# Optimization experiments

Measured on AMD Instinct MI355X. Metric: run time of the kernel, lower is better.

The kernel has to match this reference:

```python
import jax, jax.numpy as jnp
import numpy as np

UNITS = 1024
NEG_INF = -10000.0


def setup_inputs() -> dict:
    key = jax.random.key(0)
    ks = jax.random.split(key, 5)
    B, S, D = 8, 2048, 1024
    scale = 0.02  # truncated-normal stddev in original init
    x = jax.random.normal(ks[0], (B, S, D), dtype=jnp.float32)
    mask = jax.random.randint(ks[1], (B, S), 0, 2, dtype=jnp.int32)
    Wq = jax.random.normal(ks[2], (D, UNITS), dtype=jnp.float32) * scale
    Wk = jax.random.normal(ks[3], (D, UNITS), dtype=jnp.float32) * scale
    Wv = jax.random.normal(ks[4], (D, UNITS), dtype=jnp.float32) * scale
    bq = jnp.zeros((UNITS,), jnp.float32)
    bk = jnp.zeros((UNITS,), jnp.float32)
    bv = jnp.zeros((UNITS,), jnp.float32)
    return {"x": x, "mask": mask, "Wq": Wq, "bq": bq, "Wk": Wk, "bk": bk, "Wv": Wv, "bv": bv}


def reference(x, mask, Wq, bq, Wk, bk, Wv, bv):
    # Q/K/V projections: [B,S,D] @ [D,U] -> [B,S,U]
    q = jnp.einsum('bsd,du->bsu', x, Wq) + bq
    k = jnp.einsum('bsd,du->bsu', x, Wk) + bk
    v = jnp.einsum('bsd,du->bsu', x, Wv) + bv
    # scaled dot-product scores: [B,S,S]
    scores = jnp.einsum('bqu,bku->bqk', q, k) / jnp.sqrt(jnp.float32(UNITS))
    m = mask.astype(jnp.float32)
    attn_mask = jnp.einsum('bq,bk->bqk', m, m)  # outer-product padding mask
    scores = scores + (1.0 - attn_mask) * NEG_INF
    probs = jax.nn.softmax(scores, axis=-1)
    # dropout is inactive at inference (training=None/False in Keras)
    context = jnp.einsum('bqk,bku->bqu', probs, v)
    return context
```

## Files before the change

kernel.cpp:

```cpp
#include <hip/hip_runtime.h>
#include <stdint.h>

typedef unsigned short u16;
typedef __bf16 bf16x8 __attribute__((ext_vector_type(8)));
typedef float f32x4 __attribute__((ext_vector_type(4)));
typedef unsigned short u16x8 __attribute__((ext_vector_type(8)));
typedef unsigned short u16x4 __attribute__((ext_vector_type(4)));

#define B_BATCH 8
#define S_LEN   2048
#define D_DIM   1024
#define U_DIM   1024

#define BM 128
#define BN 128
#define BK 64

__device__ __forceinline__ float bf2f(u16 h) {
    union { unsigned u; float f; } c; c.u = ((unsigned)h) << 16; return c.f;
}
__device__ __forceinline__ u16 f2bf(float f) {
    union { float f; unsigned u; } c; c.f = f;
    unsigned r = c.u + 0x7fffu + ((c.u >> 16) & 1u);
    return (u16)(r >> 16);
}

__device__ __forceinline__ void cp16(u16* lds, const u16* g) {
    __builtin_amdgcn_global_load_lds((__attribute__((address_space(1))) void*)g,
                                     (__attribute__((address_space(3))) void*)lds,
                                     16, 0, 0);
}

__device__ __forceinline__ void gemm_core(
    const u16* __restrict__ A, int lda,
    const u16* __restrict__ Bt, int ldb,
    int m0, int n0, int K,
    u16* As, u16* Bs, int tid, f32x4 acc[4][4])
{
    const int lane = tid & 63;
    const int wm = ((tid >> 6) >> 1) * 64;
    const int wn = ((tid >> 6) & 1) * 64;
    const int lm = lane & 15;
    const int lq = lane >> 4;
    const int sw = lm & 7;

    for (int k0 = 0; k0 < K; k0 += BK) {
        __syncthreads();
        #pragma unroll
        for (int s = 0; s < 4; ++s) {
            const int c = tid + 256 * s;
            const int r = c >> 3;
            const int q = (c & 7) ^ ((c >> 3) & 7);
            cp16(As + c * 8, A + (long long)(m0 + r) * lda + k0 + q * 8);
            cp16(Bs + c * 8, Bt + (long long)(n0 + r) * ldb + k0 + q * 8);
        }
        __syncthreads();

        #pragma unroll
        for (int ks = 0; ks < 2; ++ks) {
            const int kq = ks * 4 + lq;
            bf16x8 af[4], bfr[4];
            #pragma unroll
            for (int i = 0; i < 4; ++i)
                af[i] = *(const bf16x8*)(As + (wm + i * 16 + lm) * BK + (kq ^ sw) * 8);
            #pragma unroll
            for (int j = 0; j < 4; ++j)
                bfr[j] = *(const bf16x8*)(Bs + (wn + j * 16 + lm) * BK + (kq ^ sw) * 8);
            #pragma unroll
            for (int i = 0; i < 4; ++i)
                #pragma unroll
                for (int j = 0; j < 4; ++j)
                    acc[i][j] = __builtin_amdgcn_mfma_f32_16x16x32_bf16(af[i], bfr[j], acc[i][j], 0, 0, 0);
        }
    }
}

__device__ __forceinline__ void swizzle_mnz(int ph, int& mi, int& ni, int& z) {
    const int lid = blockIdx.x + gridDim.x * (blockIdx.y + gridDim.y * blockIdx.z);
    z = lid & 7;
    const int t = lid >> 3;
    const int ntn = gridDim.x;
    const int panel = t / (ph * ntn);
    const int r = t - panel * (ph * ntn);
    mi = panel * ph + (r % ph);
    ni = r / ph;
}

__global__ __launch_bounds__(256) void prep(
    const float* __restrict__ x, u16* __restrict__ xb,
    const float* __restrict__ Wq, const float* __restrict__ Wk,
    const float* __restrict__ Wv, u16* __restrict__ WT,
    float* __restrict__ rowsum)
{
    __shared__ u16 tile[32][33];
    const int b = blockIdx.x;
    const int tid = threadIdx.x;
    if (b < 16384) {
        const int i = b * 256 + tid;
        float4 v = ((const float4*)x)[i];
        ushort4 o;
        o.x = f2bf(v.x); o.y = f2bf(v.y); o.z = f2bf(v.z); o.w = f2bf(v.w);
        ((ushort4*)xb)[i] = o;
    } else if (b < 16384 + 3072) {
        const int b2 = b - 16384;
        const int w = b2 >> 10;
        const int idx = b2 & 1023;
        const float* src = (w == 0) ? Wq : (w == 1) ? Wk : Wv;
        u16* dst = WT + (size_t)w * D_DIM * U_DIM;
        const int c0 = (idx & 31) * 32, rr0 = (idx >> 5) * 32;
        const int tx = tid & 31, ty = tid >> 5;
        #pragma unroll
        for (int i = 0; i < 32; i += 8)
            tile[ty + i][tx] = f2bf(src[(long long)(rr0 + ty + i) * U_DIM + c0 + tx]);
        __syncthreads();
        #pragma unroll
        for (int i = 0; i < 32; i += 8)
            dst[(long long)(c0 + ty + i) * D_DIM + rr0 + tx] = tile[tx][ty + i];
    } else {
        const int i = (b - 16384 - 3072) * 256 + tid;
        float4 z4; z4.x = z4.y = z4.z = z4.w = 0.0f;
        ((float4*)rowsum)[i] = z4;
    }
}

__global__ __launch_bounds__(256, 2) void qkv_proj(
    const u16* __restrict__ xb, const u16* __restrict__ WT,
    const float* __restrict__ bq, const float* __restrict__ bk,
    const float* __restrict__ bv,
    u16* __restrict__ Q, u16* __restrict__ Ko, u16* __restrict__ VT)
{
    __shared__ __align__(16) u16 smem[BM * BK * 2];
    u16* As = smem;
    u16* Bs = smem + BM * BK;

    const int tgt = blockIdx.x >> 3;
    const int n0 = (blockIdx.x & 7) * BN;
    const int m0 = blockIdx.y * BM;
    const int tid = threadIdx.x;
    const int lane = tid & 63;
    const int wm = ((tid >> 6) >> 1) * 64;
    const int wn = ((tid >> 6) & 1) * 64;

    const u16* Bt = WT + (size_t)tgt * (D_DIM * U_DIM);
    const float* bias = (tgt == 0) ? bq : (tgt == 1) ? bk : bv;

    f32x4 acc[4][4] = {};
    gemm_core(xb, D_DIM, Bt, D_DIM, m0, n0, D_DIM, As, Bs, tid, acc);

    const int col = lane & 15;
    const int rb  = (lane >> 4) * 4;

    if (tgt < 2) {
        u16* C = (tgt == 0) ? Q : Ko;
        #pragma unroll
        for (int j = 0; j < 4; ++j) {
            const int n = n0 + wn + j * 16 + col;
            const float bvv = bias[n];
            #pragma unroll
            for (int i = 0; i < 4; ++i) {
                const long long mr = m0 + wm + i * 16 + rb;
                #pragma unroll
                for (int r = 0; r < 4; ++r)
                    C[(mr + r) * U_DIM + n] = f2bf(acc[i][j][r] + bvv);
            }
        }
    } else {
        __syncthreads();
        #pragma unroll
        for (int j = 0; j < 4; ++j) {
            const int cl = wn + j * 16 + col;
            const float bvv = bias[n0 + cl];
            #pragma unroll
            for (int i = 0; i < 4; ++i) {
                const int rowb = wm + i * 16 + rb;
                u16x4 pk;
                #pragma unroll
                for (int r = 0; r < 4; ++r) pk[r] = f2bf(acc[i][j][r] + bvv);
                const int idx = cl * 128 + (((rowb >> 3) ^ (cl & 15)) * 8) + (rowb & 7);
                *(u16x4*)(smem + idx) = pk;
            }
        }
        __syncthreads();
        const int zb = m0 >> 11;
        const int s0 = m0 & 2047;
        u16* VTg = VT + (size_t)zb * ((size_t)S_LEN * U_DIM);
        #pragma unroll
        for (int s = 0; s < 8; ++s) {
            const int cid = tid + 256 * s;
            const int cl = cid >> 4;
            const int m8 = cid & 15;
            u16x8 v = *(const u16x8*)(smem + cl * 128 + ((m8 ^ (cl & 15)) * 8));
            *(u16x8*)(VTg + (size_t)(n0 + cl) * S_LEN + s0 + m8 * 8) = v;
        }
    }
}

__global__ __launch_bounds__(256, 2) void scores_exp(
    const u16* __restrict__ Qb, const u16* __restrict__ Kb,
    u16* __restrict__ E, const int* __restrict__ mask,
    float* __restrict__ rowsum, int ph)
{
    __shared__ __align__(16) u16 smem[BM * BK * 2];
    u16* As = smem;
    u16* Bs = smem + BM * BK;

    int mi, ni, z;
    swizzle_mnz(ph, mi, ni, z);
    const int m0 = mi * BM, n0 = ni * BN;
    const long long SU = (long long)S_LEN * U_DIM;
    const long long SS = (long long)S_LEN * S_LEN;

    const int tid = threadIdx.x;
    const int lane = tid & 63;
    const int wm = ((tid >> 6) >> 1) * 64;
    const int wn = ((tid >> 6) & 1) * 64;

    f32x4 acc[4][4] = {};
    gemm_core(Qb + (long long)z * SU, U_DIM, Kb + (long long)z * SU, U_DIM,
              m0, n0, U_DIM, As, Bs, tid, acc);

    u16* Eg = E + (long long)z * SS;
    const int* mrow = mask + (size_t)z * S_LEN;
    const int col = lane & 15;
    const int rb  = (lane >> 4) * 4;

    int mj[4];
    #pragma unroll
    for (int j = 0; j < 4; ++j) mj[j] = mrow[n0 + wn + j * 16 + col];

    #pragma unroll
    for (int i = 0; i < 4; ++i) {
        #pragma unroll
        for (int r = 0; r < 4; ++r) {
            const int row = m0 + wm + i * 16 + rb + r;
            const int mi_ = mrow[row];
            float partial = 0.0f;
            #pragma unroll
            for (int j = 0; j < 4; ++j) {
                float e = (mi_ && !mj[j]) ? 0.0f : __expf(acc[i][j][r] * 0.03125f);
                const u16 h = f2bf(e);
                Eg[(long long)row * S_LEN + n0 + wn + j * 16 + col] = h;
                partial += bf2f(h);
            }
            partial += __shfl_xor(partial, 1, 64);
            partial += __shfl_xor(partial, 2, 64);
            partial += __shfl_xor(partial, 4, 64);
            partial += __shfl_xor(partial, 8, 64);
            if ((lane & 15) == 0)
                atomicAdd(&rowsum[(size_t)z * S_LEN + row], partial);
        }
    }
}

__global__ __launch_bounds__(256, 2) void pv_gemm(
    const u16* __restrict__ E, const u16* __restrict__ VT,
    float* __restrict__ out, const float* __restrict__ rowsum, int ph)
{
    __shared__ __align__(16) u16 smem[BM * BK * 2];
    u16* As = smem;
    u16* Bs = smem + BM * BK;

    int mi, ni, z;
    swizzle_mnz(ph, mi, ni, z);
    const int m0 = mi * BM, n0 = ni * BN;
    const long long SU = (long long)S_LEN * U_DIM;
    const long long SS = (long long)S_LEN * S_LEN;

    const int tid = threadIdx.x;
    const int lane = tid & 63;
    const int wm = ((tid >> 6) >> 1) * 64;
    const int wn = ((tid >> 6) & 1) * 64;

    f32x4 acc[4][4] = {};
    gemm_core(E + (long long)z * SS, S_LEN, VT + (long long)z * SU, S_LEN,
              m0, n0, S_LEN, As, Bs, tid, acc);

    float* Cg = out + (long long)z * SU;
    const float* rs = rowsum + (size_t)z * S_LEN;
    const int col = lane & 15;
    const int rb  = (lane >> 4) * 4;

    #pragma unroll
    for (int i = 0; i < 4; ++i) {
        #pragma unroll
        for (int r = 0; r < 4; ++r) {
            const int row = m0 + wm + i * 16 + rb + r;
            const float inv = 1.0f / rs[row];
            #pragma unroll
            for (int j = 0; j < 4; ++j)
                Cg[(long long)row * U_DIM + n0 + wn + j * 16 + col] = acc[i][j][r] * inv;
        }
    }
}

extern "C" void kernel_launch(void* const* d_in, const int* in_sizes, int n_in,
                              void* d_out, int out_size, void* d_ws, size_t ws_size,
                              hipStream_t stream)
{
    (void)in_sizes; (void)n_in; (void)out_size; (void)ws_size;
    const float* x    = (const float*)d_in[0];
    const int*   mask = (const int*)d_in[1];
    const float* Wq   = (const float*)d_in[2];
    const float* bq   = (const float*)d_in[3];
    const float* Wk   = (const float*)d_in[4];
    const float* bk   = (const float*)d_in[5];
    const float* Wv   = (const float*)d_in[6];
    const float* bv   = (const float*)d_in[7];

    const size_t DU  = (size_t)D_DIM * U_DIM;
    const size_t BSU = (size_t)B_BATCH * S_LEN * U_DIM;

    u16* ws  = (u16*)d_ws;
    u16* Qb  = ws;
    u16* Kb  = Qb + BSU;
    u16* VTb = Kb + BSU;
    u16* WT  = VTb + BSU;
    float* rowsum = (float*)(WT + 3 * DU);
    u16* E   = (u16*)(rowsum + (size_t)B_BATCH * S_LEN);
    u16* xb  = E;

    dim3 blk(256);

    prep<<<dim3(16384 + 3072 + 16), blk, 0, stream>>>(x, xb, Wq, Wk, Wv, WT, rowsum);

    qkv_proj<<<dim3(24, 128), blk, 0, stream>>>(xb, WT, bq, bk, bv, Qb, Kb, VTb);

    scores_exp<<<dim3(S_LEN / BN, S_LEN / BM, B_BATCH), blk, 0, stream>>>(
        Qb, Kb, E, mask, rowsum, 8);

    pv_gemm<<<dim3(U_DIM / BN, S_LEN / BM, B_BATCH), blk, 0, stream>>>(
        E, VTb, (float*)d_out, rowsum, 16);
}
```

Baseline: 281.1 us.

## Switch GEMMs to 256x256 tiles with 8 waves and double-buffered LDS prefetch

Replaces the 128x128 single-buffered GEMM core with a 256x256-tile, 512-thread version used by all three GEMM kernels. It double-buffers the K tiles in LDS, issuing the next tile's global-to-LDS copies while the current MFMA quarters run. It splits each k-step into four MFMA quadrants separated by raw barriers and raises wave priority during the MFMA bursts. The larger tile cuts global and LDS traffic per FLOP. In exchange it uses 128KB of LDS and 128 accumulator registers per thread, which limits residency to one block per CU, and the smaller grids (256 blocks for pv_gemm) may leave load imbalance.

```diff
diff --git a/kernel.cpp b/kernel.cpp
--- a/kernel.cpp
+++ b/kernel.cpp
@@ -12,9 +12,10 @@
 #define D_DIM   1024
 #define U_DIM   1024
 
-#define BM 128
-#define BN 128
 #define BK 64
+#define HALF_U16  16384
+#define TILE_U16  32768
+#define LDS_U16   65536
 
 __device__ __forceinline__ float bf2f(u16 h) {
     union { unsigned u; float f; } c; c.u = ((unsigned)h) << 16; return c.f;
@@ -31,47 +32,106 @@
                                      16, 0, 0);
 }
 
-__device__ __forceinline__ void gemm_core(
+__device__ __forceinline__ void barrier_raw() { asm volatile("s_barrier" ::: "memory"); }
+
+__device__ __forceinline__ void stage4(u16* __restrict__ dst, const u16* __restrict__ src,
+                                       int ld, int row0, int kc, int tid) {
+    #pragma unroll
+    for (int s = 0; s < 4; ++s) {
+        const int c = tid + 512 * s;
+        const int r = c >> 3;
+        const int q = (c & 7) ^ (r & 7);
+        cp16(dst + c * 8, src + (long long)(row0 + r) * ld + kc + q * 8);
+    }
+}
+
+__device__ __forceinline__ void ldsA8(bf16x8* a, const u16* __restrict__ T,
+                                      int rbase, int lm, int lq, int sw) {
+    #pragma unroll
+    for (int i = 0; i < 4; ++i)
+        #pragma unroll
+        for (int ks = 0; ks < 2; ++ks)
+            a[i * 2 + ks] = *(const bf16x8*)(T + (rbase + i * 16 + lm) * BK + (((ks * 4 + lq) ^ sw) * 8));
+}
+__device__ __forceinline__ void ldsB4(bf16x8* b, const u16* __restrict__ T,
+                                      int rbase, int lm, int lq, int sw) {
+    #pragma unroll
+    for (int j = 0; j < 2; ++j)
+        #pragma unroll
+        for (int ks = 0; ks < 2; ++ks)
+            b[j * 2 + ks] = *(const bf16x8*)(T + (rbase + j * 16 + lm) * BK + (((ks * 4 + lq) ^ sw) * 8));
+}
+
+template<int I0, int J0>
+__device__ __forceinline__ void mmaq(f32x4 (*acc)[4], const bf16x8* a, const bf16x8* b) {
+    __builtin_amdgcn_s_setprio(1);
+    #pragma unroll
+    for (int i = 0; i < 4; ++i)
+        #pragma unroll
+        for (int j = 0; j < 2; ++j)
+            #pragma unroll
+            for (int ks = 0; ks < 2; ++ks)
+                acc[I0 + i][J0 + j] = __builtin_amdgcn_mfma_f32_16x16x32_bf16(
+                    a[i * 2 + ks], b[j * 2 + ks], acc[I0 + i][J0 + j], 0, 0, 0);
+    __builtin_amdgcn_s_setprio(0);
+    __builtin_amdgcn_sched_barrier(0);
+}
+
+__device__ __forceinline__ void gemm256(
     const u16* __restrict__ A, int lda,
     const u16* __restrict__ Bt, int ldb,
     int m0, int n0, int K,
-    u16* As, u16* Bs, int tid, f32x4 acc[4][4])
+    u16* lds, int tid, f32x4 (*acc)[4])
 {
     const int lane = tid & 63;
-    const int wm = ((tid >> 6) >> 1) * 64;
-    const int wn = ((tid >> 6) & 1) * 64;
-    const int lm = lane & 15;
-    const int lq = lane >> 4;
-    const int sw = lm & 7;
-
-    for (int k0 = 0; k0 < K; k0 += BK) {
-        __syncthreads();
-        #pragma unroll
-        for (int s = 0; s < 4; ++s) {
-            const int c = tid + 256 * s;
-            const int r = c >> 3;
-            const int q = (c & 7) ^ ((c >> 3) & 7);
-            cp16(As + c * 8, A + (long long)(m0 + r) * lda + k0 + q * 8);
-            cp16(Bs + c * 8, Bt + (long long)(n0 + r) * ldb + k0 + q * 8);
-        }
-        __syncthreads();
-
-        #pragma unroll
-        for (int ks = 0; ks < 2; ++ks) {
-            const int kq = ks * 4 + lq;
-            bf16x8 af[4], bfr[4];
-            #pragma unroll
-            for (int i = 0; i < 4; ++i)
-                af[i] = *(const bf16x8*)(As + (wm + i * 16 + lm) * BK + (kq ^ sw) * 8);
-            #pragma unroll
-            for (int j = 0; j < 4; ++j)
-                bfr[j] = *(const bf16x8*)(Bs + (wn + j * 16 + lm) * BK + (kq ^ sw) * 8);
-            #pragma unroll
-            for (int i = 0; i < 4; ++i)
-                #pragma unroll
-                for (int j = 0; j < 4; ++j)
-                    acc[i][j] = __builtin_amdgcn_mfma_f32_16x16x32_bf16(af[i], bfr[j], acc[i][j], 0, 0, 0);
-        }
+    const int wid  = tid >> 6;
+    const int wmh  = (wid >> 2) * 128;
+    const int wnh  = (wid & 3) * 64;
+    const int lm   = lane & 15;
+    const int lq   = lane >> 4;
+    const int sw   = lm & 7;
+
+    stage4(lds,            A,  lda, m0, 0, tid);
+    stage4(lds + HALF_U16, Bt, ldb, n0, 0, tid);
+    asm volatile("s_waitcnt vmcnt(0)" ::: "memory");
+    barrier_raw();
+
+    const int NT = K >> 6;
+    int buf = 0;
+    for (int kt = 0; kt < NT; ++kt) {
+        const u16* As  = lds + buf * TILE_U16;
+        const u16* Bs  = As + HALF_U16;
+        u16* Asn = lds + (buf ^ 1) * TILE_U16;
+        u16* Bsn = Asn + HALF_U16;
+        const int kn = (kt + 1) << 6;
+        const bool pre = (kt + 1) < NT;
+        bf16x8 a[8], b[4];
+
+        ldsA8(a, As, wmh, lm, lq, sw);
+        ldsB4(b, Bs, wnh, lm, lq, sw);
+        if (pre) stage4(Asn, A, lda, m0, kn, tid);
+        barrier_raw();
+        mmaq<0, 0>(acc, a, b);
+        barrier_raw();
+
+        ldsB4(b, Bs, wnh + 32, lm, lq, sw);
+        if (pre) stage4(Bsn, Bt, ldb, n0, kn, tid);
+        barrier_raw();
+        mmaq<0, 2>(acc, a, b);
+        barrier_raw();
+
+        ldsA8(a, As, wmh + 64, lm, lq, sw);
+        barrier_raw();
+        mmaq<4, 2>(acc, a, b);
+        barrier_raw();
+
+        ldsB4(b, Bs, wnh, lm, lq, sw);
+        if (pre) asm volatile("s_waitcnt vmcnt(0)" ::: "memory");
+        barrier_raw();
+        mmaq<4, 0>(acc, a, b);
+        barrier_raw();
+
+        buf ^= 1;
     }
 }
 
@@ -123,42 +183,36 @@
     }
 }
 
-__global__ __launch_bounds__(256, 2) void qkv_proj(
+__global__ __launch_bounds__(512, 2) void qkv_proj(
     const u16* __restrict__ xb, const u16* __restrict__ WT,
     const float* __restrict__ bq, const float* __restrict__ bk,
     const float* __restrict__ bv,
     u16* __restrict__ Q, u16* __restrict__ Ko, u16* __restrict__ VT)
 {
-    __shared__ __align__(16) u16 smem[BM * BK * 2];
-    u16* As = smem;
-    u16* Bs = smem + BM * BK;
-
-    const int tgt = blockIdx.x >> 3;
-    const int n0 = (blockIdx.x & 7) * BN;
-    const int m0 = blockIdx.y * BM;
+    __shared__ __align__(16) u16 smem[LDS_U16];
+    const int tgt = blockIdx.x >> 2;
+    const int n0 = (blockIdx.x & 3) * 256;
+    const int m0 = blockIdx.y * 256;
     const int tid = threadIdx.x;
-    const int lane = tid & 63;
-    const int wm = ((tid >> 6) >> 1) * 64;
-    const int wn = ((tid >> 6) & 1) * 64;
+    const int lane = tid & 63, wid = tid >> 6;
+    const int wmh = (wid >> 2) * 128, wnh = (wid & 3) * 64;
+    const int lm = lane & 15, lq = lane >> 4;
 
     const u16* Bt = WT + (size_t)tgt * (D_DIM * U_DIM);
     const float* bias = (tgt == 0) ? bq : (tgt == 1) ? bk : bv;
 
-    f32x4 acc[4][4] = {};
-    gemm_core(xb, D_DIM, Bt, D_DIM, m0, n0, D_DIM, As, Bs, tid, acc);
-
-    const int col = lane & 15;
-    const int rb  = (lane >> 4) * 4;
+    f32x4 acc[8][4] = {};
+    gemm256(xb, D_DIM, Bt, D_DIM, m0, n0, D_DIM, smem, tid, acc);
 
     if (tgt < 2) {
         u16* C = (tgt == 0) ? Q : Ko;
         #pragma unroll
         for (int j = 0; j < 4; ++j) {
-            const int n = n0 + wn + j * 16 + col;
+            const int n = n0 + wnh + j * 16 + lm;
             const float bvv = bias[n];
             #pragma unroll
-            for (int i = 0; i < 4; ++i) {
-                const long long mr = m0 + wm + i * 16 + rb;
+            for (int i = 0; i < 8; ++i) {
+                const long long mr = m0 + wmh + i * 16 + lq * 4;
                 #pragma unroll
                 for (int r = 0; r < 4; ++r)
                     C[(mr + r) * U_DIM + n] = f2bf(acc[i][j][r] + bvv);
@@ -168,15 +222,15 @@
         __syncthreads();
         #pragma unroll
         for (int j = 0; j < 4; ++j) {
-            const int cl = wn + j * 16 + col;
+            const int cl = wnh + j * 16 + lm;
             const float bvv = bias[n0 + cl];
             #pragma unroll
-            for (int i = 0; i < 4; ++i) {
-                const int rowb = wm + i * 16 + rb;
+            for (int i = 0; i < 8; ++i) {
+                const int rowb = wmh + i * 16 + lq * 4;
                 u16x4 pk;
                 #pragma unroll
                 for (int r = 0; r < 4; ++r) pk[r] = f2bf(acc[i][j][r] + bvv);
-                const int idx = cl * 128 + (((rowb >> 3) ^ (cl & 15)) * 8) + (rowb & 7);
+                const int idx = cl * 256 + (((rowb >> 3) ^ (cl & 31)) * 8) + (rowb & 7);
                 *(u16x4*)(smem + idx) = pk;
             }
         }
@@ -185,110 +239,102 @@
         const int s0 = m0 & 2047;
         u16* VTg = VT + (size_t)zb * ((size_t)S_LEN * U_DIM);
         #pragma unroll
-        for (int s = 0; s < 8; ++s) {
-            const int cid = tid + 256 * s;
-            const int cl = cid >> 4;
-            const int m8 = cid & 15;
-            u16x8 v = *(const u16x8*)(smem + cl * 128 + ((m8 ^ (cl & 15)) * 8));
+        for (int s = 0; s < 16; ++s) {
+            const int cid = tid + 512 * s;
+            const int cl = cid >> 5;
+            const int m8 = cid & 31;
+            u16x8 v = *(const u16x8*)(smem + cl * 256 + ((m8 ^ (cl & 31)) * 8));
             *(u16x8*)(VTg + (size_t)(n0 + cl) * S_LEN + s0 + m8 * 8) = v;
         }
     }
 }
 
-__global__ __launch_bounds__(256, 2) void scores_exp(
+__global__ __launch_bounds__(512, 2) void scores_exp(
     const u16* __restrict__ Qb, const u16* __restrict__ Kb,
     u16* __restrict__ E, const int* __restrict__ mask,
     float* __restrict__ rowsum, int ph)
 {
-    __shared__ __align__(16) u16 smem[BM * BK * 2];
-    u16* As = smem;
-    u16* Bs = smem + BM * BK;
+    __shared__ __align__(16) u16 smem[LDS_U16];
 
     int mi, ni, z;
     swizzle_mnz(ph, mi, ni, z);
-    const int m0 = mi * BM, n0 = ni * BN;
+    const int m0 = mi * 256, n0 = ni * 256;
     const long long SU = (long long)S_LEN * U_DIM;
     const long long SS = (long long)S_LEN * S_LEN;
 
     const int tid = threadIdx.x;
-    const int lane = tid & 63;
-    const int wm = ((tid >> 6) >> 1) * 64;
-    const int wn = ((tid >> 6) & 1) * 64;
-
-    f32x4 acc[4][4] = {};
-    gemm_core(Qb + (long long)z * SU, U_DIM, Kb + (long long)z * SU, U_DIM,
-              m0, n0, U_DIM, As, Bs, tid, acc);
+    const int lane = tid & 63, wid = tid >> 6;
+    const int wmh = (wid >> 2) * 128, wnh = (wid & 3) * 64;
+    const int lm = lane & 15, lq = lane >> 4;
+
+    f32x4 acc[8][4] = {};
+    gemm256(Qb + (long long)z * SU, U_DIM, Kb + (long long)z * SU, U_DIM,
+            m0, n0, U_DIM, smem, tid, acc);
 
     u16* Eg = E + (long long)z * SS;
     const int* mrow = mask + (size_t)z * S_LEN;
-    const int col = lane & 15;
-    const int rb  = (lane >> 4) * 4;
 
     int mj[4];
     #pragma unroll
-    for (int j = 0; j < 4; ++j) mj[j] = mrow[n0 + wn + j * 16 + col];
-
-    #pragma unroll
-    for (int i = 0; i < 4; ++i) {
+    for (int j = 0; j < 4; ++j) mj[j] = mrow[n0 + wnh + j * 16 + lm];
+
+    #pragma unroll
+    for (int i = 0; i < 8; ++i) {
         #pragma unroll
         for (int r = 0; r < 4; ++r) {
-            const int row = m0 + wm + i * 16 + rb + r;
+            const int row = m0 + wmh + i * 16 + lq * 4 + r;
             const int mi_ = mrow[row];
             float partial = 0.0f;
             #pragma unroll
             for (int j = 0; j < 4; ++j) {
                 float e = (mi_ && !mj[j]) ? 0.0f : __expf(acc[i][j][r] * 0.03125f);
                 const u16 h = f2bf(e);
-                Eg[(long long)row * S_LEN + n0 + wn + j * 16 + col] = h;
+                Eg[(long long)row * S_LEN + n0 + wnh + j * 16 + lm] = h;
                 partial += bf2f(h);
             }
             partial += __shfl_xor(partial, 1, 64);
             partial += __shfl_xor(partial, 2, 64);
             partial += __shfl_xor(partial, 4, 64);
             partial += __shfl_xor(partial, 8, 64);
-            if ((lane & 15) == 0)
+            if (lm == 0)
                 atomicAdd(&rowsum[(size_t)z * S_LEN + row], partial);
         }
     }
 }
 
-__global__ __launch_bounds__(256, 2) void pv_gemm(
+__global__ __launch_bounds__(512, 2) void pv_gemm(
     const u16* __restrict__ E, const u16* __restrict__ VT,
     float* __restrict__ out, const float* __restrict__ rowsum, int ph)
 {
-    __shared__ __align__(16) u16 smem[BM * BK * 2];
-    u16* As = smem;
-    u16* Bs = smem + BM * BK;
+    __shared__ __align__(16) u16 smem[LDS_U16];
 
     int mi, ni, z;
     swizzle_mnz(ph, mi, ni, z);
-    const int m0 = mi * BM, n0 = ni * BN;
+    const int m0 = mi * 256, n0 = ni * 256;
     const long long SU = (long long)S_LEN * U_DIM;
     const long long SS = (long long)S_LEN * S_LEN;
 
     const int tid = threadIdx.x;
-    const int lane = tid & 63;
-    const int wm = ((tid >> 6) >> 1) * 64;
-    const int wn = ((tid >> 6) & 1) * 64;
-
-    f32x4 acc[4][4] = {};
-    gemm_core(E + (long long)z * SS, S_LEN, VT + (long long)z * SU, S_LEN,
-              m0, n0, S_LEN, As, Bs, tid, acc);
+    const int lane = tid & 63, wid = tid >> 6;
+    const int wmh = (wid >> 2) * 128, wnh = (wid & 3) * 64;
+    const int lm = lane & 15, lq = lane >> 4;
+
+    f32x4 acc[8][4] = {};
+    gemm256(E + (long long)z * SS, S_LEN, VT + (long long)z * SU, S_LEN,
+            m0, n0, S_LEN, smem, tid, acc);
 
     float* Cg = out + (long long)z * SU;
     const float* rs = rowsum + (size_t)z * S_LEN;
-    const int col = lane & 15;
-    const int rb  = (lane >> 4) * 4;
-
-    #pragma unroll
-    for (int i = 0; i < 4; ++i) {
+
+    #pragma unroll
+    for (int i = 0; i < 8; ++i) {
         #pragma unroll
         for (int r = 0; r < 4; ++r) {
-            const int row = m0 + wm + i * 16 + rb + r;
+            const int row = m0 + wmh + i * 16 + lq * 4 + r;
             const float inv = 1.0f / rs[row];
             #pragma unroll
             for (int j = 0; j < 4; ++j)
-                Cg[(long long)row * U_DIM + n0 + wn + j * 16 + col] = acc[i][j][r] * inv;
+                Cg[(long long)row * U_DIM + n0 + wnh + j * 16 + lm] = acc[i][j][r] * inv;
         }
     }
 }
@@ -319,15 +365,11 @@
     u16* E   = (u16*)(rowsum + (size_t)B_BATCH * S_LEN);
     u16* xb  = E;
 
-    dim3 blk(256);
-
-    prep<<<dim3(16384 + 3072 + 16), blk, 0, stream>>>(x, xb, Wq, Wk, Wv, WT, rowsum);
-
-    qkv_proj<<<dim3(24, 128), blk, 0, stream>>>(xb, WT, bq, bk, bv, Qb, Kb, VTb);
-
-    scores_exp<<<dim3(S_LEN / BN, S_LEN / BM, B_BATCH), blk, 0, stream>>>(
-        Qb, Kb, E, mask, rowsum, 8);
-
-    pv_gemm<<<dim3(U_DIM / BN, S_LEN / BM, B_BATCH), blk, 0, stream>>>(
-        E, VTb, (float*)d_out, rowsum, 16);
-}
+    prep<<<dim3(16384 + 3072 + 16), dim3(256), 0, stream>>>(x, xb, Wq, Wk, Wv, WT, rowsum);
+
+    qkv_proj<<<dim3(12, 64), dim3(512), 0, stream>>>(xb, WT, bq, bk, bv, Qb, Kb, VTb);
+
+    scores_exp<<<dim3(8, 8, 8), dim3(512), 0, stream>>>(Qb, Kb, E, mask, rowsum, 8);
+
+    pv_gemm<<<dim3(4, 8, 8), dim3(512), 0, stream>>>(E, VTb, (float*)d_out, rowsum, 8);
+}
```

Measured after the change: 290.1 us. 1.03x slower.

## Enlarge GEMM block tile to 256x128 with 128-row warp tiles

Applied to the files above, without the earlier changes.

Doubles the M dimension of the block tile across all three GEMM kernels, so each wave computes a 128x64 sub-tile with 8x4 MFMA accumulators. The aim is to raise arithmetic intensity and reuse of the B fragments, cutting LDS and global traffic per FLOP. The V-transpose epilogue now goes through shared memory in two halves because the staging buffer holds only half the tile, and the swizzle panel height is adjusted. In exchange, accumulator registers double and the grid halves, which risks lower occupancy and spills.

```diff
diff --git a/kernel.cpp b/kernel.cpp
--- a/kernel.cpp
+++ b/kernel.cpp
@@ -12,7 +12,7 @@
 #define D_DIM   1024
 #define U_DIM   1024
 
-#define BM 128
+#define BM 256
 #define BN 128
 #define BK 64
 
@@ -35,10 +35,10 @@
     const u16* __restrict__ A, int lda,
     const u16* __restrict__ Bt, int ldb,
     int m0, int n0, int K,
-    u16* As, u16* Bs, int tid, f32x4 acc[4][4])
+    u16* As, u16* Bs, int tid, f32x4 acc[8][4])
 {
     const int lane = tid & 63;
-    const int wm = ((tid >> 6) >> 1) * 64;
+    const int wm = ((tid >> 6) >> 1) * 128;
     const int wn = ((tid >> 6) & 1) * 64;
     const int lm = lane & 15;
     const int lq = lane >> 4;
@@ -47,11 +47,17 @@
     for (int k0 = 0; k0 < K; k0 += BK) {
         __syncthreads();
         #pragma unroll
+        for (int s = 0; s < 8; ++s) {
+            const int c = tid + 256 * s;
+            const int r = c >> 3;
+            const int q = (c & 7) ^ (r & 7);
+            cp16(As + c * 8, A + (long long)(m0 + r) * lda + k0 + q * 8);
+        }
+        #pragma unroll
         for (int s = 0; s < 4; ++s) {
             const int c = tid + 256 * s;
             const int r = c >> 3;
-            const int q = (c & 7) ^ ((c >> 3) & 7);
-            cp16(As + c * 8, A + (long long)(m0 + r) * lda + k0 + q * 8);
+            const int q = (c & 7) ^ (r & 7);
             cp16(Bs + c * 8, Bt + (long long)(n0 + r) * ldb + k0 + q * 8);
         }
         __syncthreads();
@@ -59,18 +65,17 @@
         #pragma unroll
         for (int ks = 0; ks < 2; ++ks) {
             const int kq = ks * 4 + lq;
-            bf16x8 af[4], bfr[4];
-            #pragma unroll
-            for (int i = 0; i < 4; ++i)
-                af[i] = *(const bf16x8*)(As + (wm + i * 16 + lm) * BK + (kq ^ sw) * 8);
+            bf16x8 bfr[4];
             #pragma unroll
             for (int j = 0; j < 4; ++j)
-                bfr[j] = *(const bf16x8*)(Bs + (wn + j * 16 + lm) * BK + (kq ^ sw) * 8);
-            #pragma unroll
-            for (int i = 0; i < 4; ++i)
+                bfr[j] = *(const bf16x8*)(Bs + (wn + j * 16 + lm) * BK + ((kq ^ sw) * 8));
+            #pragma unroll
+            for (int i = 0; i < 8; ++i) {
+                const bf16x8 af = *(const bf16x8*)(As + (wm + i * 16 + lm) * BK + ((kq ^ sw) * 8));
                 #pragma unroll
                 for (int j = 0; j < 4; ++j)
-                    acc[i][j] = __builtin_amdgcn_mfma_f32_16x16x32_bf16(af[i], bfr[j], acc[i][j], 0, 0, 0);
+                    acc[i][j] = __builtin_amdgcn_mfma_f32_16x16x32_bf16(af, bfr[j], acc[i][j], 0, 0, 0);
+            }
         }
     }
 }
@@ -129,7 +134,7 @@
     const float* __restrict__ bv,
     u16* __restrict__ Q, u16* __restrict__ Ko, u16* __restrict__ VT)
 {
-    __shared__ __align__(16) u16 smem[BM * BK * 2];
+    __shared__ __align__(16) u16 smem[(BM + BN) * BK];
     u16* As = smem;
     u16* Bs = smem + BM * BK;
 
@@ -138,13 +143,13 @@
     const int m0 = blockIdx.y * BM;
     const int tid = threadIdx.x;
     const int lane = tid & 63;
-    const int wm = ((tid >> 6) >> 1) * 64;
+    const int wm = ((tid >> 6) >> 1) * 128;
     const int wn = ((tid >> 6) & 1) * 64;
 
     const u16* Bt = WT + (size_t)tgt * (D_DIM * U_DIM);
     const float* bias = (tgt == 0) ? bq : (tgt == 1) ? bk : bv;
 
-    f32x4 acc[4][4] = {};
+    f32x4 acc[8][4] = {};
     gemm_core(xb, D_DIM, Bt, D_DIM, m0, n0, D_DIM, As, Bs, tid, acc);
 
     const int col = lane & 15;
@@ -157,7 +162,7 @@
             const int n = n0 + wn + j * 16 + col;
             const float bvv = bias[n];
             #pragma unroll
-            for (int i = 0; i < 4; ++i) {
+            for (int i = 0; i < 8; ++i) {
                 const long long mr = m0 + wm + i * 16 + rb;
                 #pragma unroll
                 for (int r = 0; r < 4; ++r)
@@ -165,32 +170,38 @@
             }
         }
     } else {
-        __syncthreads();
-        #pragma unroll
-        for (int j = 0; j < 4; ++j) {
-            const int cl = wn + j * 16 + col;
-            const float bvv = bias[n0 + cl];
-            #pragma unroll
-            for (int i = 0; i < 4; ++i) {
-                const int rowb = wm + i * 16 + rb;
-                u16x4 pk;
-                #pragma unroll
-                for (int r = 0; r < 4; ++r) pk[r] = f2bf(acc[i][j][r] + bvv);
-                const int idx = cl * 128 + (((rowb >> 3) ^ (cl & 15)) * 8) + (rowb & 7);
-                *(u16x4*)(smem + idx) = pk;
-            }
-        }
-        __syncthreads();
         const int zb = m0 >> 11;
         const int s0 = m0 & 2047;
         u16* VTg = VT + (size_t)zb * ((size_t)S_LEN * U_DIM);
-        #pragma unroll
-        for (int s = 0; s < 8; ++s) {
-            const int cid = tid + 256 * s;
-            const int cl = cid >> 4;
-            const int m8 = cid & 15;
-            u16x8 v = *(const u16x8*)(smem + cl * 128 + ((m8 ^ (cl & 15)) * 8));
-            *(u16x8*)(VTg + (size_t)(n0 + cl) * S_LEN + s0 + m8 * 8) = v;
+        const int hw = (tid >> 6) >> 1;
+        #pragma unroll
+        for (int h = 0; h < 2; ++h) {
+            __syncthreads();
+            if (hw == h) {
+                #pragma unroll
+                for (int j = 0; j < 4; ++j) {
+                    const int cl = wn + j * 16 + col;
+                    const float bvv = bias[n0 + cl];
+                    #pragma unroll
+                    for (int i = 0; i < 8; ++i) {
+                        const int rowb = i * 16 + rb;
+                        u16x4 pk;
+                        #pragma unroll
+                        for (int r = 0; r < 4; ++r) pk[r] = f2bf(acc[i][j][r] + bvv);
+                        const int idx = cl * 128 + (((rowb >> 3) ^ (cl & 15)) * 8) + (rowb & 7);
+                        *(u16x4*)(smem + idx) = pk;
+                    }
+                }
+            }
+            __syncthreads();
+            #pragma unroll
+            for (int s = 0; s < 8; ++s) {
+                const int cid = tid + 256 * s;
+                const int cl = cid >> 4;
+                const int m8 = cid & 15;
+                u16x8 v = *(const u16x8*)(smem + cl * 128 + ((m8 ^ (cl & 15)) * 8));
+                *(u16x8*)(VTg + (size_t)(n0 + cl) * S_LEN + s0 + h * 128 + m8 * 8) = v;
+            }
         }
     }
 }
@@ -200,7 +211,7 @@
     u16* __restrict__ E, const int* __restrict__ mask,
     float* __restrict__ rowsum, int ph)
 {
-    __shared__ __align__(16) u16 smem[BM * BK * 2];
+    __shared__ __align__(16) u16 smem[(BM + BN) * BK];
     u16* As = smem;
     u16* Bs = smem + BM * BK;
 
@@ -212,10 +223,10 @@
 
     const int tid = threadIdx.x;
     const int lane = tid & 63;
-    const int wm = ((tid >> 6) >> 1) * 64;
+    const int wm = ((tid >> 6) >> 1) * 128;
     const int wn = ((tid >> 6) & 1) * 64;
 
-    f32x4 acc[4][4] = {};
+    f32x4 acc[8][4] = {};
     gemm_core(Qb + (long long)z * SU, U_DIM, Kb + (long long)z * SU, U_DIM,
               m0, n0, U_DIM, As, Bs, tid, acc);
 
@@ -229,7 +240,7 @@
     for (int j = 0; j < 4; ++j) mj[j] = mrow[n0 + wn + j * 16 + col];
 
     #pragma unroll
-    for (int i = 0; i < 4; ++i) {
+    for (int i = 0; i < 8; ++i) {
         #pragma unroll
         for (int r = 0; r < 4; ++r) {
             const int row = m0 + wm + i * 16 + rb + r;
@@ -256,7 +267,7 @@
     const u16* __restrict__ E, const u16* __restrict__ VT,
     float* __restrict__ out, const float* __restrict__ rowsum, int ph)
 {
-    __shared__ __align__(16) u16 smem[BM * BK * 2];
+    __shared__ __align__(16) u16 smem[(BM + BN) * BK];
     u16* As = smem;
     u16* Bs = smem + BM * BK;
 
@@ -268,10 +279,10 @@
 
     const int tid = threadIdx.x;
     const int lane = tid & 63;
-    const int wm = ((tid >> 6) >> 1) * 64;
+    const int wm = ((tid >> 6) >> 1) * 128;
     const int wn = ((tid >> 6) & 1) * 64;
 
-    f32x4 acc[4][4] = {};
+    f32x4 acc[8][4] = {};
     gemm_core(E + (long long)z * SS, S_LEN, VT + (long long)z * SU, S_LEN,
               m0, n0, S_LEN, As, Bs, tid, acc);
 
@@ -281,7 +292,7 @@
     const int rb  = (lane >> 4) * 4;
 
     #pragma unroll
-    for (int i = 0; i < 4; ++i) {
+    for (int i = 0; i < 8; ++i) {
         #pragma unroll
         for (int r = 0; r < 4; ++r) {
             const int row = m0 + wm + i * 16 + rb + r;
@@ -323,11 +334,11 @@
 
     prep<<<dim3(16384 + 3072 + 16), blk, 0, stream>>>(x, xb, Wq, Wk, Wv, WT, rowsum);
 
-    qkv_proj<<<dim3(24, 128), blk, 0, stream>>>(xb, WT, bq, bk, bv, Qb, Kb, VTb);
+    qkv_proj<<<dim3(24, 64), blk, 0, stream>>>(xb, WT, bq, bk, bv, Qb, Kb, VTb);
 
     scores_exp<<<dim3(S_LEN / BN, S_LEN / BM, B_BATCH), blk, 0, stream>>>(
         Qb, Kb, E, mask, rowsum, 8);
 
     pv_gemm<<<dim3(U_DIM / BN, S_LEN / BM, B_BATCH), blk, 0, stream>>>(
-        E, VTb, (float*)d_out, rowsum, 16);
-}
+        E, VTb, (float*)d_out, rowsum, 8);
+}
```

Result: no change. 284.9 us (+1.3%).
